# Optimization experiments

Hardware: AMD Instinct MI355X
Metric: run time of the kernel (lower is better)

The kernel has to match this reference:

```python
import jax, jax.numpy as jnp
import numpy as np

B, N, C = 8, 2048, 128
K = 16
DILATIONS = (1, 2)
KMAX = K * max(DILATIONS)  # neighbors constructed by DilatedKnnGraph
NEG_SLOPE = 0.2


def setup_inputs() -> dict:
    key = jax.random.key(0)
    ks = jax.random.split(key, 12)
    D = len(DILATIONS)

    def nrm(k, shape, fan_in):
        return jax.random.normal(k, shape, jnp.float32) / np.float32(np.sqrt(fan_in))

    x = jax.random.normal(ks[0], (B, N, C), jnp.float32)
    pos = jax.random.normal(ks[1], (B, N, 3), jnp.float32)
    # PointTransformerConv params per dilation layer (bias-free lin/lin_src/lin_dst, pos_nn=Linear(3,C))
    W_lin = nrm(ks[2], (D, C, C), C)
    W_src = nrm(ks[3], (D, C, C), C)
    W_dst = nrm(ks[4], (D, C, C), C)
    W_pos = nrm(ks[5], (D, 3, C), 3)
    b_pos = jnp.zeros((D, C), jnp.float32)
    # global fusion MLP: Linear(C+3, C) + LeakyReLU(0.2)
    Wg = nrm(ks[6], (C + 3, C), C + 3)
    bg = jnp.zeros((C,), jnp.float32)
    # final MLP: Linear(C,C) + LeakyReLU(0.2) + Linear(C,3)
    W1 = nrm(ks[7], (C, C), C)
    b1 = jnp.zeros((C,), jnp.float32)
    W2 = nrm(ks[8], (C, 3), C)
    b2 = jnp.zeros((3,), jnp.float32)
    return dict(x=x, pos=pos, W_lin=W_lin, W_src=W_src, W_dst=W_dst,
                W_pos=W_pos, b_pos=b_pos, Wg=Wg, bg=bg, W1=W1, b1=b1, W2=W2, b2=b2)


def _knn(p):
    # p: [N, 3] -> [N, KMAX] neighbor indices sorted by ascending distance (self excluded)
    sq = jnp.sum(p * p, axis=-1)
    d2 = sq[:, None] + sq[None, :] - 2.0 * (p @ p.T)
    d2 = d2 + jnp.eye(p.shape[0], dtype=p.dtype) * jnp.float32(1e10)
    _, idx = jax.lax.top_k(-d2, KMAX)
    return idx


def reference(x, pos, W_lin, W_src, W_dst, W_pos, b_pos, Wg, bg, W1, b1, W2, b2):
    nbr = jax.vmap(_knn)(pos)  # [B, N, KMAX]
    self_idx = jnp.broadcast_to(jnp.arange(N)[None, :, None], (B, N, 1))
    gather = jax.vmap(lambda arr, idx: arr[idx])  # per-cloud fancy gather

    h = None
    for li, d in enumerate(DILATIONS):
        # Dilated neighbor selection: every d-th of sorted neighbors, keep K, plus self loop
        idx = jnp.concatenate([nbr[:, :, ::d][:, :, :K], self_idx], axis=-1)  # [B, N, K+1]
        pos_j = gather(pos, idx)  # [B, N, K+1, 3]
        # delta_ij = pos_nn(pos_i - pos_j)
        delta = jnp.einsum('bnkt,tc->bnkc', pos[:, :, None, :] - pos_j, W_pos[li]) + b_pos[li]
        s = x @ W_src[li]   # lin_src
        v = x @ W_lin[li]   # value projection
        t = x @ W_dst[li]   # lin_dst
        # alpha_ij = lin_dst(x_i) - lin_src(x_j) + delta ; per-channel softmax over neighbors
        alpha = t[:, :, None, :] - gather(s, idx) + delta  # [B, N, K+1, C]
        w = jax.nn.softmax(alpha, axis=2)
        h_ = jnp.sum(w * (gather(v, idx) + delta), axis=2)  # [B, N, C]
        h = h_ if h is None else h + h_

    h2 = jax.nn.leaky_relu(jnp.concatenate([x, pos], axis=-1) @ Wg + bg, NEG_SLOPE)
    h = h + h2
    res = jax.nn.leaky_relu(h @ W1 + b1, NEG_SLOPE) @ W2 + b2
    return res + pos  # add_points=True
```

## Files before the change

kernel.cpp:

```cpp
#include <hip/hip_runtime.h>

#define BB 8
#define NN 2048
#define CC 128
#define KMAX 32
#define NEG 0.2f
#define CH 8
#define CHSZ (NN / CH)
#define CAP 32

using bf16x8 = __attribute__((ext_vector_type(8))) short;
using f32x4  = __attribute__((ext_vector_type(4))) float;

__device__ __forceinline__ unsigned int f2key(float f) {
  unsigned int b = __float_as_uint(f);
  return (b & 0x80000000u) ? ~b : (b | 0x80000000u);
}

__device__ __forceinline__ float sq3(float x, float y, float z) {
  return __fadd_rn(__fadd_rn(__fmul_rn(x, x), __fmul_rn(y, y)), __fmul_rn(z, z));
}

__device__ __forceinline__ float d2np(float px, float py, float pz, float sqq,
                                      float qx, float qy, float qz, float sqj) {
  float dot = __fmaf_rn(pz, qz, __fmaf_rn(py, qy, __fmul_rn(px, qx)));
  return __fsub_rn(__fadd_rn(sqq, sqj), __fmul_rn(2.0f, dot));
}

__device__ __forceinline__ unsigned short f2bf(float f) {
  unsigned int u = __float_as_uint(f);
  return (unsigned short)((u + 0x7fffu + ((u >> 16) & 1u)) >> 16);
}
__device__ __forceinline__ float bf2f(unsigned short u) {
  return __uint_as_float(((unsigned int)u) << 16);
}

__device__ __forceinline__ bf16x8 cvt8(const float* __restrict__ p) {
  float4 a = *(const float4*)(p);
  float4 b = *(const float4*)(p + 4);
  bf16x8 r;
  r[0] = (short)f2bf(a.x); r[1] = (short)f2bf(a.y);
  r[2] = (short)f2bf(a.z); r[3] = (short)f2bf(a.w);
  r[4] = (short)f2bf(b.x); r[5] = (short)f2bf(b.y);
  r[6] = (short)f2bf(b.z); r[7] = (short)f2bf(b.w);
  return r;
}

__device__ __forceinline__ int paddr(int c, int jj) { return (c << 8) + (jj ^ c); }

__device__ __forceinline__ void knn_body(int bx, int tid,
                                         const float* __restrict__ pos,
                                         unsigned short* __restrict__ cand,
                                         unsigned int* __restrict__ candk,
                                         float4* __restrict__ sp4,
                                         unsigned char* __restrict__ sbuf) {
  int b = bx >> 6;
  int qbase = (bx & 63) * 32;
  const float* pb = pos + (size_t)b * NN * 3;
  for (int t = tid; t < NN; t += 256) {
    float xx = pb[t * 3 + 0];
    float yy = pb[t * 3 + 1];
    float zz = pb[t * 3 + 2];
    sp4[paddr(t >> 8, t & 255)] = make_float4(xx, yy, zz, sq3(xx, yy, zz));
  }
  __syncthreads();

  int q = qbase + (tid >> 3);
  int c = tid & 7;
  float4 pq = sp4[paddr(q >> 8, q & 255)];
  float px = pq.x, py = pq.y, pz = pq.z;
  float sqq = pq.w;
  int j0 = c * CHSZ;

  const float SENT = 3.0e38f;
  float a0 = SENT, a1 = SENT, a2 = SENT, a3 = SENT;
#pragma unroll 4
  for (int jj = 0; jj < CHSZ; ++jj) {
    float4 pj = sp4[paddr(c, jj)];
    float d2 = d2np(px, py, pz, sqq, pj.x, pj.y, pj.z, pj.w);
    if (j0 + jj == q) d2 = SENT;
    float m0 = fmaxf(a0, d2); a0 = fminf(a0, d2);
    float m1 = fmaxf(a1, m0); a1 = fminf(a1, m0);
    float m2 = fmaxf(a2, m1); a2 = fminf(a2, m1);
    a3 = fminf(a3, m2);
  }

  float T = a3;
  T = fmaxf(T, __shfl_xor(T, 1));
  T = fmaxf(T, __shfl_xor(T, 2));
  T = fmaxf(T, __shfl_xor(T, 4));

  unsigned int ak[KMAX];
  int ai[KMAX];
#pragma unroll
  for (int k = 0; k < KMAX; ++k) { ak[k] = 0xFFFFFFFFu; ai[k] = 0xFFFF; }

  int sbase = tid * CAP;
  auto drain = [&](int cnt2) {
    for (int u = 0; u < cnt2; ++u) {
      int jj2 = (int)sbuf[sbase + u];
      int j = j0 + jj2;
      float4 pj = sp4[paddr(c, jj2)];
      float d2 = d2np(px, py, pz, sqq, pj.x, pj.y, pj.z, pj.w);
      unsigned int key = f2key(d2);
      if (key < ak[KMAX - 1]) {
#pragma unroll
        for (int k = KMAX - 1; k >= 1; --k) {
          bool ck  = key < ak[k];
          bool ckm = key < ak[k - 1];
          unsigned int tk = ckm ? ak[k - 1] : key;
          int          ti = ckm ? ai[k - 1] : j;
          ak[k] = ck ? tk : ak[k];
          ai[k] = ck ? ti : ai[k];
        }
        bool c0b = key < ak[0];
        ak[0] = c0b ? key : ak[0];
        ai[0] = c0b ? j : ai[0];
      }
    }
  };

  int cnt = 0;
  for (int jj = 0; jj < CHSZ; ++jj) {
    float4 pj = sp4[paddr(c, jj)];
    float d2 = d2np(px, py, pz, sqq, pj.x, pj.y, pj.z, pj.w);
    bool pass = (d2 <= T) && (j0 + jj != q);
    if (pass) {
      if (cnt == CAP) { drain(CAP); cnt = 0; }
      sbuf[sbase + cnt] = (unsigned char)jj;
      ++cnt;
    }
  }
  drain(cnt);

  size_t obase = (((size_t)(b * NN + q)) * CH + c) * KMAX;
  unsigned short* oc = cand + obase;
  unsigned int* ok = candk + obase;
#pragma unroll
  for (int k = 0; k < KMAX; ++k) {
    oc[k] = (unsigned short)ai[k];
    ok[k] = ak[k];
  }
}

__device__ __forceinline__ void proj_body(int z, int mx, int tid,
                                          const float* __restrict__ x,
                                          const unsigned short* __restrict__ wf,
                                          unsigned short* __restrict__ projb) {
  unsigned short* out = projb + (size_t)z * ((size_t)BB * NN * CC);
  int wave = tid >> 6;
  int lane = tid & 63;
  int m0 = (mx * 4 + wave) * 16;
  int quad = lane >> 4;
  int am = m0 + (lane & 15);

  f32x4 acc[8];
#pragma unroll
  for (int nt = 0; nt < 8; ++nt) acc[nt] = (f32x4){0.f, 0.f, 0.f, 0.f};

  const unsigned short* wz = wf + (size_t)z * (8 * 4 * 64 * 8);
#pragma unroll
  for (int ks = 0; ks < 4; ++ks) {
    bf16x8 a = cvt8(x + (size_t)am * CC + ks * 32 + quad * 8);
#pragma unroll
    for (int nt = 0; nt < 8; ++nt) {
      bf16x8 bfr = *(const bf16x8*)(wz + (size_t)(((nt * 4 + ks) * 64 + lane) * 8));
      acc[nt] = __builtin_amdgcn_mfma_f32_16x16x32_bf16(a, bfr, acc[nt], 0, 0, 0);
    }
  }

  int col0 = lane & 15;
#pragma unroll
  for (int nt = 0; nt < 8; ++nt)
#pragma unroll
    for (int r = 0; r < 4; ++r)
      out[(size_t)(m0 + quad * 4 + r) * CC + nt * 16 + col0] = f2bf(acc[nt][r]);
}

__device__ __forceinline__ void wg_body(int mx, int tid,
                                        const float* __restrict__ x,
                                        const float* __restrict__ pos,
                                        const unsigned short* __restrict__ wf,
                                        const float* __restrict__ wgtail,
                                        const float* __restrict__ bg,
                                        float* __restrict__ h) {
  int wave = tid >> 6;
  int lane = tid & 63;
  int m0 = (mx * 4 + wave) * 16;
  int quad = lane >> 4;
  int am = m0 + (lane & 15);

  f32x4 acc[8];
#pragma unroll
  for (int nt = 0; nt < 8; ++nt) acc[nt] = (f32x4){0.f, 0.f, 0.f, 0.f};

  const unsigned short* wz = wf + (size_t)6 * (8 * 4 * 64 * 8);
#pragma unroll
  for (int ks = 0; ks < 4; ++ks) {
    bf16x8 a = cvt8(x + (size_t)am * CC + ks * 32 + quad * 8);
#pragma unroll
    for (int nt = 0; nt < 8; ++nt) {
      bf16x8 b = *(const bf16x8*)(wz + (size_t)(((nt * 4 + ks) * 64 + lane) * 8));
      acc[nt] = __builtin_amdgcn_mfma_f32_16x16x32_bf16(a, b, acc[nt], 0, 0, 0);
    }
  }

  float posr[4][3];
#pragma unroll
  for (int r = 0; r < 4; ++r) {
    int m = m0 + quad * 4 + r;
    posr[r][0] = pos[m * 3 + 0];
    posr[r][1] = pos[m * 3 + 1];
    posr[r][2] = pos[m * 3 + 2];
  }

  int col0 = lane & 15;
#pragma unroll
  for (int nt = 0; nt < 8; ++nt) {
    int col = nt * 16 + col0;
    float bv = bg[col];
    float t0 = wgtail[col];
    float t1 = wgtail[CC + col];
    float t2 = wgtail[2 * CC + col];
#pragma unroll
    for (int r = 0; r < 4; ++r) {
      float v = acc[nt][r] + bv
              + posr[r][0] * t0 + posr[r][1] * t1 + posr[r][2] * t2;
      v = v > 0.f ? v : NEG * v;
      h[(size_t)(m0 + quad * 4 + r) * CC + col] = v;
    }
  }
}

__global__ __launch_bounds__(256) void fused_front(
    const float* __restrict__ pos,
    unsigned short* __restrict__ cand,
    unsigned int* __restrict__ candk,
    const float* __restrict__ x,
    const unsigned short* __restrict__ wf,
    unsigned short* __restrict__ projb,
    const float* __restrict__ wgtail,
    const float* __restrict__ bg,
    float* __restrict__ h) {
  __shared__ float4 sp4[CH * 256];
  __shared__ unsigned char sbuf[256 * CAP];

  if (blockIdx.x < 512) {
    knn_body(blockIdx.x, threadIdx.x, pos, cand, candk, sp4, sbuf);
  } else if (blockIdx.x < 2048) {
    int bx = blockIdx.x - 512;
    proj_body(bx >> 8, bx & 255, threadIdx.x, x, wf, projb);
  } else {
    wg_body(blockIdx.x - 2048, threadIdx.x, x, pos, wf, wgtail, bg, h);
  }
}

__global__ __launch_bounds__(256) void knn_p1(const float* __restrict__ pos,
                                              unsigned short* __restrict__ cand,
                                              unsigned int* __restrict__ candk) {
  __shared__ float4 sp4[CH * 256];
  __shared__ unsigned char sbuf[256 * CAP];
  knn_body(blockIdx.x, threadIdx.x, pos, cand, candk, sp4, sbuf);
}

__global__ __launch_bounds__(64) void knn_p2(const unsigned int* __restrict__ candk,
                                             const unsigned short* __restrict__ cand,
                                             int* __restrict__ nbr) {
  int q = blockIdx.x * 64 + threadIdx.x;
  const unsigned int* k8 = candk + (size_t)q * (CH * KMAX);
  const unsigned short* i8 = cand + (size_t)q * (CH * KMAX);

  int head[CH];
  unsigned int hk[CH];
#pragma unroll
  for (int c = 0; c < CH; ++c) {
    head[c] = 0;
    hk[c] = k8[c * KMAX];
  }

  int* onb = nbr + (size_t)q * KMAX;
#pragma unroll
  for (int r = 0; r < KMAX; ++r) {
    int bc = 0;
    unsigned int bk = hk[0];
#pragma unroll
    for (int c = 1; c < CH; ++c) {
      if (hk[c] < bk) { bk = hk[c]; bc = c; }
    }
    onb[r] = (int)i8[bc * KMAX + head[bc]];
    ++head[bc];
    hk[bc] = (head[bc] < KMAX) ? k8[bc * KMAX + head[bc]] : 0xFFFFFFFFu;
  }
}

__global__ __launch_bounds__(256) void wcvt(const float* __restrict__ Wa,
                                            const float* __restrict__ Wb,
                                            const float* __restrict__ Wc,
                                            const float* __restrict__ Wgm,
                                            const float* __restrict__ W1m,
                                            unsigned short* __restrict__ wf) {
  int t = blockIdx.x * 256 + threadIdx.x;
  int lane = t & 63;
  int ks = (t >> 6) & 3;
  int nt = (t >> 8) & 7;
  int z = t >> 11;
  const float* W = (z < 2) ? (Wa + (size_t)z * CC * CC)
                 : (z < 4) ? (Wb + (size_t)(z - 2) * CC * CC)
                 : (z < 6) ? (Wc + (size_t)(z - 4) * CC * CC)
                 : (z == 6) ? Wgm : W1m;
  int n = nt * 16 + (lane & 15);
  int kb = ks * 32 + (lane >> 4) * 8;
  unsigned short* o = wf + (size_t)t * 8;
#pragma unroll
  for (int j = 0; j < 8; ++j)
    o[j] = f2bf(W[(size_t)(kb + j) * CC + n]);
}

__global__ __launch_bounds__(256) void proj_fly(const float* __restrict__ x,
                                                const unsigned short* __restrict__ wf,
                                                unsigned short* __restrict__ projb) {
  proj_body(blockIdx.z, blockIdx.x, threadIdx.x, x, wf, projb);
}
__global__ __launch_bounds__(256) void wg_fly(const float* __restrict__ x,
                                              const float* __restrict__ pos,
                                              const unsigned short* __restrict__ wf,
                                              const float* __restrict__ wgtail,
                                              const float* __restrict__ bg,
                                              float* __restrict__ h) {
  wg_body(blockIdx.x, threadIdx.x, x, pos, wf, wgtail, bg, h);
}

__global__ __launch_bounds__(128) void attn2_kernel(
    const float* __restrict__ pos, const int* __restrict__ nbr,
    const unsigned short* __restrict__ s0, const unsigned short* __restrict__ v0,
    const unsigned short* __restrict__ t0,
    const unsigned short* __restrict__ s1, const unsigned short* __restrict__ v1,
    const unsigned short* __restrict__ t1,
    const float* __restrict__ Wpos, const float* __restrict__ bpos,
    const float* __restrict__ h, unsigned short* __restrict__ hb) {
  int b = blockIdx.x & 7;
  int n = blockIdx.x >> 3;
  int bn = (b << 11) + n;
  int c = threadIdx.x;

  const float* pb = pos + (size_t)b * NN * 3;
  float pix = pb[n * 3 + 0], piy = pb[n * 3 + 1], piz = pb[n * 3 + 2];

  const int* nb = nbr + (size_t)bn * KMAX;
  int idxs[KMAX];
#pragma unroll
  for (int u = 0; u < KMAX / 4; ++u) {
    int4 v4 = *(const int4*)(nb + u * 4);
    idxs[u * 4 + 0] = v4.x; idxs[u * 4 + 1] = v4.y;
    idxs[u * 4 + 2] = v4.z; idxs[u * 4 + 3] = v4.w;
  }

  float ht = h[(size_t)bn * CC + c];

#pragma unroll
  for (int l = 0; l < 2; ++l) {
    int dil = l + 1;
    const unsigned short* s = l ? s1 : s0;
    const unsigned short* v = l ? v1 : v0;
    const unsigned short* t = l ? t1 : t0;
    const float* Wp = Wpos + (size_t)l * 3 * CC;
    float w0 = Wp[c], w1 = Wp[CC + c], w2 = Wp[2 * CC + c];
    float bp = bpos[(size_t)l * CC + c];
    float tc = bf2f(t[(size_t)bn * CC + c]);

    int id[17];
#pragma unroll
    for (int j = 0; j < 17; ++j) id[j] = (j < 16) ? idxs[j * dil] : n;

    float sc[17];
#pragma unroll
    for (int j = 0; j < 17; ++j)
      sc[j] = bf2f(s[((size_t)(b * NN + id[j])) * CC + c]);

    float alpha[17], del[17];
#pragma unroll
    for (int j = 0; j < 17; ++j) {
      int idx = id[j];
      float dx = pix - pb[idx * 3 + 0];
      float dy = piy - pb[idx * 3 + 1];
      float dz = piz - pb[idx * 3 + 2];
      float d = dx * w0 + dy * w1 + dz * w2 + bp;
      del[j] = d;
      alpha[j] = tc - sc[j] + d;
    }
    float m8[8];
#pragma unroll
    for (int j = 0; j < 8; ++j) m8[j] = fmaxf(alpha[j], alpha[j + 8]);
    float m4a = fmaxf(m8[0], m8[1]), m4b = fmaxf(m8[2], m8[3]);
    float m4c = fmaxf(m8[4], m8[5]), m4d = fmaxf(m8[6], m8[7]);
    float mx = fmaxf(fmaxf(fmaxf(m4a, m4b), fmaxf(m4c, m4d)), alpha[16]);

    float sum = 0.f;
#pragma unroll
    for (int j = 0; j < 17; ++j) {
      float w = __expf(alpha[j] - mx);
      alpha[j] = w;
      sum += w;
    }
    float inv = 1.f / sum;

    float vc[17];
#pragma unroll
    for (int j = 0; j < 17; ++j)
      vc[j] = bf2f(v[((size_t)(b * NN + id[j])) * CC + c]);

    float hc = 0.f;
#pragma unroll
    for (int j = 0; j < 17; ++j)
      hc += alpha[j] * (vc[j] + del[j]);
    ht += hc * inv;
  }

  hb[(size_t)bn * CC + c] = f2bf(ht);
}

__global__ __launch_bounds__(256) void mfma_w1_final(
    const unsigned short* __restrict__ hb,
    const unsigned short* __restrict__ wz,
    const float* __restrict__ b1,
    const float* __restrict__ W2,
    const float* __restrict__ b2,
    const float* __restrict__ pos,
    float* __restrict__ out) {
  int wave = threadIdx.x >> 6;
  int lane = threadIdx.x & 63;
  int m0 = (blockIdx.x * 4 + wave) * 16;
  int quad = lane >> 4;
  int am = m0 + (lane & 15);

  f32x4 acc[8];
#pragma unroll
  for (int nt = 0; nt < 8; ++nt) acc[nt] = (f32x4){0.f, 0.f, 0.f, 0.f};

#pragma unroll
  for (int ks = 0; ks < 4; ++ks) {
    bf16x8 a = *(const bf16x8*)(hb + (size_t)am * CC + ks * 32 + quad * 8);
#pragma unroll
    for (int nt = 0; nt < 8; ++nt) {
      bf16x8 b = *(const bf16x8*)(wz + (size_t)(((nt * 4 + ks) * 64 + lane) * 8));
      acc[nt] = __builtin_amdgcn_mfma_f32_16x16x32_bf16(a, b, acc[nt], 0, 0, 0);
    }
  }

  int col0 = lane & 15;
  float part[4][3];
#pragma unroll
  for (int r = 0; r < 4; ++r)
#pragma unroll
    for (int d = 0; d < 3; ++d) part[r][d] = 0.f;

#pragma unroll
  for (int nt = 0; nt < 8; ++nt) {
    int col = nt * 16 + col0;
    float bv = b1[col];
    float w20 = W2[col * 3 + 0];
    float w21 = W2[col * 3 + 1];
    float w22 = W2[col * 3 + 2];
#pragma unroll
    for (int r = 0; r < 4; ++r) {
      float gv = acc[nt][r] + bv;
      gv = gv > 0.f ? gv : NEG * gv;
      part[r][0] = fmaf(gv, w20, part[r][0]);
      part[r][1] = fmaf(gv, w21, part[r][1]);
      part[r][2] = fmaf(gv, w22, part[r][2]);
    }
  }

#pragma unroll
  for (int off = 8; off >= 1; off >>= 1) {
#pragma unroll
    for (int r = 0; r < 4; ++r)
#pragma unroll
      for (int d = 0; d < 3; ++d)
        part[r][d] += __shfl_xor(part[r][d], off);
  }

  if (col0 == 0) {
#pragma unroll
    for (int r = 0; r < 4; ++r) {
      int m = m0 + quad * 4 + r;
#pragma unroll
      for (int d = 0; d < 3; ++d)
        out[(size_t)m * 3 + d] = part[r][d] + b2[d] + pos[(size_t)m * 3 + d];
    }
  }
}

extern "C" void kernel_launch(void* const* d_in, const int* in_sizes, int n_in,
                              void* d_out, int out_size, void* d_ws, size_t ws_size,
                              hipStream_t stream) {
  const float* x     = (const float*)d_in[0];
  const float* pos   = (const float*)d_in[1];
  const float* W_lin = (const float*)d_in[2];
  const float* W_src = (const float*)d_in[3];
  const float* W_dst = (const float*)d_in[4];
  const float* W_pos = (const float*)d_in[5];
  const float* b_pos = (const float*)d_in[6];
  const float* Wg    = (const float*)d_in[7];
  const float* bg    = (const float*)d_in[8];
  const float* W1    = (const float*)d_in[9];
  const float* b1    = (const float*)d_in[10];
  const float* W2    = (const float*)d_in[11];
  const float* b2    = (const float*)d_in[12];
  float* out = (float*)d_out;

  const size_t M = (size_t)BB * NN;
  const size_t MC = M * CC;

  char* ws = (char*)d_ws;
  int* nbr = (int*)ws;
  unsigned short* cand = (unsigned short*)(ws + M * KMAX * sizeof(int));
  float* fb = (float*)(ws + M * KMAX * sizeof(int) + M * CH * KMAX * sizeof(unsigned short));
  unsigned short* projb = (unsigned short*)fb;
  unsigned short* sb0 = projb + 0 * MC;
  unsigned short* sb1 = projb + 1 * MC;
  unsigned short* vb0 = projb + 2 * MC;
  unsigned short* vb1 = projb + 3 * MC;
  unsigned short* tb0 = projb + 4 * MC;
  unsigned short* tb1 = projb + 5 * MC;
  unsigned int* candk = (unsigned int*)(fb + 3 * MC);
  float* h = fb + 5 * MC;

  const size_t BASE = M * KMAX * sizeof(int) + M * CH * KMAX * sizeof(unsigned short)
                    + 8 * MC * sizeof(float);
  const size_t XB_BYTES = MC * sizeof(unsigned short);
  const size_t WF_BYTES = 8 * 16384 * sizeof(unsigned short);
  const size_t FRAG = (size_t)(8 * 4 * 64 * 8);
  bool fused_ok = ws_size >= BASE + XB_BYTES + WF_BYTES;

  if (fused_ok) {
    unsigned short* hb = (unsigned short*)(ws + BASE);
    unsigned short* wf = (unsigned short*)(ws + BASE + XB_BYTES);

    wcvt<<<64, 256, 0, stream>>>(W_src, W_lin, W_dst, Wg, W1, wf);
    fused_front<<<2304, 256, 0, stream>>>(pos, cand, candk, x, wf, projb,
                                          Wg + 128 * CC, bg, h);
    knn_p2<<<256, 64, 0, stream>>>(candk, cand, nbr);
    attn2_kernel<<<M, 128, 0, stream>>>(pos, nbr, sb0, vb0, tb0,
                                        sb1, vb1, tb1, W_pos, b_pos, h, hb);
    mfma_w1_final<<<M / 64, 256, 0, stream>>>(hb, wf + 7 * FRAG, b1,
                                              W2, b2, pos, out);
  } else {
    unsigned short* hb = cand;
    unsigned short* wf = cand + MC;
    knn_p1<<<512, 256, 0, stream>>>(pos, cand, candk);
    knn_p2<<<256, 64, 0, stream>>>(candk, cand, nbr);
    wcvt<<<64, 256, 0, stream>>>(W_src, W_lin, W_dst, Wg, W1, wf);
    proj_fly<<<dim3(256, 1, 6), 256, 0, stream>>>(x, wf, projb);
    wg_fly<<<256, 256, 0, stream>>>(x, pos, wf, Wg + 128 * CC, bg, h);
    attn2_kernel<<<M, 128, 0, stream>>>(pos, nbr, sb0, vb0, tb0,
                                        sb1, vb1, tb1, W_pos, b_pos, h, hb);
    mfma_w1_final<<<M / 64, 256, 0, stream>>>(hb, wf + 7 * FRAG, b1,
                                              W2, b2, pos, out);
  }
}
```

Baseline: 218.6 us.

## Fuse kNN candidate merge into kNN kernel and precompute per-point pos projections

The per-chunk kNN candidate lists are now merged inside the kNN block through shared memory, with one thread per query. This removes the separate knn_p2 launch and the global round-trip of the candidate keys and indices. Separately, pos@W_pos is precomputed once per point and layer into an fp32 buffer in an enlarged wcvt kernel. The attention kernel then forms delta as the difference of two gathered projection rows instead of recomputing it from three gathered coordinates. The precompute exploits linearity to drop per-edge FMAs, but it adds a 16 MB fp32 buffer and many wide per-neighbor gathers. The in-block merge runs serially on only one thread in eight.

```diff
diff --git a/kernel.cpp b/kernel.cpp
--- a/kernel.cpp
+++ b/kernel.cpp
@@ -50,8 +50,7 @@
 
 __device__ __forceinline__ void knn_body(int bx, int tid,
                                          const float* __restrict__ pos,
-                                         unsigned short* __restrict__ cand,
-                                         unsigned int* __restrict__ candk,
+                                         int* __restrict__ nbr,
                                          float4* __restrict__ sp4,
                                          unsigned char* __restrict__ sbuf) {
   int b = bx >> 6;
@@ -133,13 +132,37 @@
   }
   drain(cnt);
 
-  size_t obase = (((size_t)(b * NN + q)) * CH + c) * KMAX;
-  unsigned short* oc = cand + obase;
-  unsigned int* ok = candk + obase;
+  __syncthreads();
+  unsigned int* mkey = (unsigned int*)sp4;
+  unsigned char* mjj = sbuf;
+  int ql = tid >> 3;
+  int mbase = (ql * 8 + c) * 32;
 #pragma unroll
   for (int k = 0; k < KMAX; ++k) {
-    oc[k] = (unsigned short)ai[k];
-    ok[k] = ak[k];
+    mkey[mbase + k] = ak[k];
+    mjj[mbase + k] = (unsigned char)(ai[k] & 255);
+  }
+  __syncthreads();
+  if (c == 0) {
+    unsigned int hk[CH];
+    int hd[CH];
+#pragma unroll
+    for (int cc = 0; cc < CH; ++cc) {
+      hd[cc] = 0;
+      hk[cc] = mkey[(ql * 8 + cc) * 32];
+    }
+    int* onb = nbr + ((size_t)(b * NN + q)) * KMAX;
+    for (int r = 0; r < KMAX; ++r) {
+      int bc = 0;
+      unsigned int bk = hk[0];
+#pragma unroll
+      for (int cc = 1; cc < CH; ++cc) {
+        if (hk[cc] < bk) { bk = hk[cc]; bc = cc; }
+      }
+      onb[r] = bc * CHSZ + (int)mjj[(ql * 8 + bc) * 32 + hd[bc]];
+      ++hd[bc];
+      hk[bc] = (hd[bc] < KMAX) ? mkey[(ql * 8 + bc) * 32 + hd[bc]] : 0xFFFFFFFFu;
+    }
   }
 }
 
@@ -234,8 +257,7 @@
 
 __global__ __launch_bounds__(256) void fused_front(
     const float* __restrict__ pos,
-    unsigned short* __restrict__ cand,
-    unsigned int* __restrict__ candk,
+    int* __restrict__ nbr,
     const float* __restrict__ x,
     const unsigned short* __restrict__ wf,
     unsigned short* __restrict__ projb,
@@ -246,7 +268,7 @@
   __shared__ unsigned char sbuf[256 * CAP];
 
   if (blockIdx.x < 512) {
-    knn_body(blockIdx.x, threadIdx.x, pos, cand, candk, sp4, sbuf);
+    knn_body(blockIdx.x, threadIdx.x, pos, nbr, sp4, sbuf);
   } else if (blockIdx.x < 2048) {
     int bx = blockIdx.x - 512;
     proj_body(bx >> 8, bx & 255, threadIdx.x, x, wf, projb);
@@ -256,41 +278,10 @@
 }
 
 __global__ __launch_bounds__(256) void knn_p1(const float* __restrict__ pos,
-                                              unsigned short* __restrict__ cand,
-                                              unsigned int* __restrict__ candk) {
+                                              int* __restrict__ nbr) {
   __shared__ float4 sp4[CH * 256];
   __shared__ unsigned char sbuf[256 * CAP];
-  knn_body(blockIdx.x, threadIdx.x, pos, cand, candk, sp4, sbuf);
-}
-
-__global__ __launch_bounds__(64) void knn_p2(const unsigned int* __restrict__ candk,
-                                             const unsigned short* __restrict__ cand,
-                                             int* __restrict__ nbr) {
-  int q = blockIdx.x * 64 + threadIdx.x;
-  const unsigned int* k8 = candk + (size_t)q * (CH * KMAX);
-  const unsigned short* i8 = cand + (size_t)q * (CH * KMAX);
-
-  int head[CH];
-  unsigned int hk[CH];
-#pragma unroll
-  for (int c = 0; c < CH; ++c) {
-    head[c] = 0;
-    hk[c] = k8[c * KMAX];
-  }
-
-  int* onb = nbr + (size_t)q * KMAX;
-#pragma unroll
-  for (int r = 0; r < KMAX; ++r) {
-    int bc = 0;
-    unsigned int bk = hk[0];
-#pragma unroll
-    for (int c = 1; c < CH; ++c) {
-      if (hk[c] < bk) { bk = hk[c]; bc = c; }
-    }
-    onb[r] = (int)i8[bc * KMAX + head[bc]];
-    ++head[bc];
-    hk[bc] = (head[bc] < KMAX) ? k8[bc * KMAX + head[bc]] : 0xFFFFFFFFu;
-  }
+  knn_body(blockIdx.x, threadIdx.x, pos, nbr, sp4, sbuf);
 }
 
 __global__ __launch_bounds__(256) void wcvt(const float* __restrict__ Wa,
@@ -298,22 +289,42 @@
                                             const float* __restrict__ Wc,
                                             const float* __restrict__ Wgm,
                                             const float* __restrict__ W1m,
-                                            unsigned short* __restrict__ wf) {
-  int t = blockIdx.x * 256 + threadIdx.x;
-  int lane = t & 63;
-  int ks = (t >> 6) & 3;
-  int nt = (t >> 8) & 7;
-  int z = t >> 11;
-  const float* W = (z < 2) ? (Wa + (size_t)z * CC * CC)
-                 : (z < 4) ? (Wb + (size_t)(z - 2) * CC * CC)
-                 : (z < 6) ? (Wc + (size_t)(z - 4) * CC * CC)
-                 : (z == 6) ? Wgm : W1m;
-  int n = nt * 16 + (lane & 15);
-  int kb = ks * 32 + (lane >> 4) * 8;
-  unsigned short* o = wf + (size_t)t * 8;
-#pragma unroll
-  for (int j = 0; j < 8; ++j)
-    o[j] = f2bf(W[(size_t)(kb + j) * CC + n]);
+                                            unsigned short* __restrict__ wf,
+                                            const float* __restrict__ Wpos,
+                                            const float* __restrict__ pos,
+                                            float* __restrict__ pp) {
+  if (blockIdx.x < 64) {
+    int t = blockIdx.x * 256 + threadIdx.x;
+    int lane = t & 63;
+    int ks = (t >> 6) & 3;
+    int nt = (t >> 8) & 7;
+    int z = t >> 11;
+    const float* W = (z < 2) ? (Wa + (size_t)z * CC * CC)
+                   : (z < 4) ? (Wb + (size_t)(z - 2) * CC * CC)
+                   : (z < 6) ? (Wc + (size_t)(z - 4) * CC * CC)
+                   : (z == 6) ? Wgm : W1m;
+    int n = nt * 16 + (lane & 15);
+    int kb = ks * 32 + (lane >> 4) * 8;
+    unsigned short* o = wf + (size_t)t * 8;
+#pragma unroll
+    for (int j = 0; j < 8; ++j)
+      o[j] = f2bf(W[(size_t)(kb + j) * CC + n]);
+  } else {
+    int pb2 = blockIdx.x - 64;
+    int l = threadIdx.x >> 7;
+    int c = threadIdx.x & 127;
+    const float* Wp = Wpos + (size_t)l * 3 * CC;
+    float w0 = Wp[c], w1 = Wp[CC + c], w2 = Wp[2 * CC + c];
+    float* ppl = pp + (size_t)l * ((size_t)BB * NN * CC);
+    int m0 = pb2 * 128;
+    for (int mi = 0; mi < 128; ++mi) {
+      int m = m0 + mi;
+      float xx = pos[m * 3 + 0];
+      float yy = pos[m * 3 + 1];
+      float zz = pos[m * 3 + 2];
+      ppl[(size_t)m * CC + c] = __fmaf_rn(zz, w2, __fmaf_rn(yy, w1, __fmul_rn(xx, w0)));
+    }
+  }
 }
 
 __global__ __launch_bounds__(256) void proj_fly(const float* __restrict__ x,
@@ -331,21 +342,18 @@
 }
 
 __global__ __launch_bounds__(128) void attn2_kernel(
-    const float* __restrict__ pos, const int* __restrict__ nbr,
+    const int* __restrict__ nbr,
     const unsigned short* __restrict__ s0, const unsigned short* __restrict__ v0,
     const unsigned short* __restrict__ t0,
     const unsigned short* __restrict__ s1, const unsigned short* __restrict__ v1,
     const unsigned short* __restrict__ t1,
-    const float* __restrict__ Wpos, const float* __restrict__ bpos,
+    const float* __restrict__ pp, const float* __restrict__ bpos,
     const float* __restrict__ h, unsigned short* __restrict__ hb) {
   int b = blockIdx.x & 7;
   int n = blockIdx.x >> 3;
   int bn = (b << 11) + n;
   int c = threadIdx.x;
 
-  const float* pb = pos + (size_t)b * NN * 3;
-  float pix = pb[n * 3 + 0], piy = pb[n * 3 + 1], piz = pb[n * 3 + 2];
-
   const int* nb = nbr + (size_t)bn * KMAX;
   int idxs[KMAX];
 #pragma unroll
@@ -363,28 +371,27 @@
     const unsigned short* s = l ? s1 : s0;
     const unsigned short* v = l ? v1 : v0;
     const unsigned short* t = l ? t1 : t0;
-    const float* Wp = Wpos + (size_t)l * 3 * CC;
-    float w0 = Wp[c], w1 = Wp[CC + c], w2 = Wp[2 * CC + c];
+    const float* ppl = pp + (size_t)l * ((size_t)BB * NN * CC);
     float bp = bpos[(size_t)l * CC + c];
     float tc = bf2f(t[(size_t)bn * CC + c]);
+    float ppi = ppl[(size_t)bn * CC + c];
 
     int id[17];
 #pragma unroll
     for (int j = 0; j < 17; ++j) id[j] = (j < 16) ? idxs[j * dil] : n;
 
-    float sc[17];
+    float sc[17], pj[17];
 #pragma unroll
     for (int j = 0; j < 17; ++j)
       sc[j] = bf2f(s[((size_t)(b * NN + id[j])) * CC + c]);
+#pragma unroll
+    for (int j = 0; j < 17; ++j)
+      pj[j] = ppl[((size_t)(b * NN + id[j])) * CC + c];
 
     float alpha[17], del[17];
 #pragma unroll
     for (int j = 0; j < 17; ++j) {
-      int idx = id[j];
-      float dx = pix - pb[idx * 3 + 0];
-      float dy = piy - pb[idx * 3 + 1];
-      float dz = piz - pb[idx * 3 + 2];
-      float d = dx * w0 + dy * w1 + dz * w2 + bp;
+      float d = ppi - pj[j] + bp;
       del[j] = d;
       alpha[j] = tc - sc[j] + d;
     }
@@ -523,8 +530,8 @@
   unsigned short* vb1 = projb + 3 * MC;
   unsigned short* tb0 = projb + 4 * MC;
   unsigned short* tb1 = projb + 5 * MC;
-  unsigned int* candk = (unsigned int*)(fb + 3 * MC);
   float* h = fb + 5 * MC;
+  float* pp = fb + 6 * MC;
 
   const size_t BASE = M * KMAX * sizeof(int) + M * CH * KMAX * sizeof(unsigned short)
                     + 8 * MC * sizeof(float);
@@ -537,24 +544,22 @@
     unsigned short* hb = (unsigned short*)(ws + BASE);
     unsigned short* wf = (unsigned short*)(ws + BASE + XB_BYTES);
 
-    wcvt<<<64, 256, 0, stream>>>(W_src, W_lin, W_dst, Wg, W1, wf);
-    fused_front<<<2304, 256, 0, stream>>>(pos, cand, candk, x, wf, projb,
+    wcvt<<<192, 256, 0, stream>>>(W_src, W_lin, W_dst, Wg, W1, wf, W_pos, pos, pp);
+    fused_front<<<2304, 256, 0, stream>>>(pos, nbr, x, wf, projb,
                                           Wg + 128 * CC, bg, h);
-    knn_p2<<<256, 64, 0, stream>>>(candk, cand, nbr);
-    attn2_kernel<<<M, 128, 0, stream>>>(pos, nbr, sb0, vb0, tb0,
-                                        sb1, vb1, tb1, W_pos, b_pos, h, hb);
+    attn2_kernel<<<M, 128, 0, stream>>>(nbr, sb0, vb0, tb0,
+                                        sb1, vb1, tb1, pp, b_pos, h, hb);
     mfma_w1_final<<<M / 64, 256, 0, stream>>>(hb, wf + 7 * FRAG, b1,
                                               W2, b2, pos, out);
   } else {
     unsigned short* hb = cand;
     unsigned short* wf = cand + MC;
-    knn_p1<<<512, 256, 0, stream>>>(pos, cand, candk);
-    knn_p2<<<256, 64, 0, stream>>>(candk, cand, nbr);
-    wcvt<<<64, 256, 0, stream>>>(W_src, W_lin, W_dst, Wg, W1, wf);
+    knn_p1<<<512, 256, 0, stream>>>(pos, nbr);
+    wcvt<<<192, 256, 0, stream>>>(W_src, W_lin, W_dst, Wg, W1, wf, W_pos, pos, pp);
     proj_fly<<<dim3(256, 1, 6), 256, 0, stream>>>(x, wf, projb);
     wg_fly<<<256, 256, 0, stream>>>(x, pos, wf, Wg + 128 * CC, bg, h);
-    attn2_kernel<<<M, 128, 0, stream>>>(pos, nbr, sb0, vb0, tb0,
-                                        sb1, vb1, tb1, W_pos, b_pos, h, hb);
+    attn2_kernel<<<M, 128, 0, stream>>>(nbr, sb0, vb0, tb0,
+                                        sb1, vb1, tb1, pp, b_pos, h, hb);
     mfma_w1_final<<<M / 64, 256, 0, stream>>>(hb, wf + 7 * FRAG, b1,
                                               W2, b2, pos, out);
   }
```

Measured after the change: 214.9 us. Within noise of the previous version (-1.7%).

## Precompute per-point positional projections and gather them in attention kernel

Applied to the files above, without the earlier changes.

Uses linearity of pos_nn to precompute pos@W_pos per point and layer in fp32 inside the weight-conversion kernel (extra blocks). The attention kernel then gathers these 128-channel projections per neighbor instead of 3 position floats and computing dot products. This replaces cheap arithmetic with large fp32 gathers (17 per layer per channel), adding 16 MB writes and much more gather traffic. It also changes rounding order slightly.

```diff
diff --git a/kernel.cpp b/kernel.cpp
--- a/kernel.cpp
+++ b/kernel.cpp
@@ -298,22 +298,42 @@
                                             const float* __restrict__ Wc,
                                             const float* __restrict__ Wgm,
                                             const float* __restrict__ W1m,
-                                            unsigned short* __restrict__ wf) {
-  int t = blockIdx.x * 256 + threadIdx.x;
-  int lane = t & 63;
-  int ks = (t >> 6) & 3;
-  int nt = (t >> 8) & 7;
-  int z = t >> 11;
-  const float* W = (z < 2) ? (Wa + (size_t)z * CC * CC)
-                 : (z < 4) ? (Wb + (size_t)(z - 2) * CC * CC)
-                 : (z < 6) ? (Wc + (size_t)(z - 4) * CC * CC)
-                 : (z == 6) ? Wgm : W1m;
-  int n = nt * 16 + (lane & 15);
-  int kb = ks * 32 + (lane >> 4) * 8;
-  unsigned short* o = wf + (size_t)t * 8;
-#pragma unroll
-  for (int j = 0; j < 8; ++j)
-    o[j] = f2bf(W[(size_t)(kb + j) * CC + n]);
+                                            unsigned short* __restrict__ wf,
+                                            const float* __restrict__ Wpos,
+                                            const float* __restrict__ pos,
+                                            float* __restrict__ pp) {
+  if (blockIdx.x < 64) {
+    int t = blockIdx.x * 256 + threadIdx.x;
+    int lane = t & 63;
+    int ks = (t >> 6) & 3;
+    int nt = (t >> 8) & 7;
+    int z = t >> 11;
+    const float* W = (z < 2) ? (Wa + (size_t)z * CC * CC)
+                   : (z < 4) ? (Wb + (size_t)(z - 2) * CC * CC)
+                   : (z < 6) ? (Wc + (size_t)(z - 4) * CC * CC)
+                   : (z == 6) ? Wgm : W1m;
+    int n = nt * 16 + (lane & 15);
+    int kb = ks * 32 + (lane >> 4) * 8;
+    unsigned short* o = wf + (size_t)t * 8;
+#pragma unroll
+    for (int j = 0; j < 8; ++j)
+      o[j] = f2bf(W[(size_t)(kb + j) * CC + n]);
+  } else {
+    int pb2 = blockIdx.x - 64;
+    int l = threadIdx.x >> 7;
+    int c = threadIdx.x & 127;
+    const float* Wp = Wpos + (size_t)l * 3 * CC;
+    float w0 = Wp[c], w1 = Wp[CC + c], w2 = Wp[2 * CC + c];
+    float* ppl = pp + (size_t)l * ((size_t)BB * NN * CC);
+    int m0 = pb2 * 128;
+    for (int mi = 0; mi < 128; ++mi) {
+      int m = m0 + mi;
+      float xx = pos[m * 3 + 0];
+      float yy = pos[m * 3 + 1];
+      float zz = pos[m * 3 + 2];
+      ppl[(size_t)m * CC + c] = __fmaf_rn(zz, w2, __fmaf_rn(yy, w1, __fmul_rn(xx, w0)));
+    }
+  }
 }
 
 __global__ __launch_bounds__(256) void proj_fly(const float* __restrict__ x,
@@ -331,21 +351,18 @@
 }
 
 __global__ __launch_bounds__(128) void attn2_kernel(
-    const float* __restrict__ pos, const int* __restrict__ nbr,
+    const int* __restrict__ nbr,
     const unsigned short* __restrict__ s0, const unsigned short* __restrict__ v0,
     const unsigned short* __restrict__ t0,
     const unsigned short* __restrict__ s1, const unsigned short* __restrict__ v1,
     const unsigned short* __restrict__ t1,
-    const float* __restrict__ Wpos, const float* __restrict__ bpos,
+    const float* __restrict__ pp, const float* __restrict__ bpos,
     const float* __restrict__ h, unsigned short* __restrict__ hb) {
   int b = blockIdx.x & 7;
   int n = blockIdx.x >> 3;
   int bn = (b << 11) + n;
   int c = threadIdx.x;
 
-  const float* pb = pos + (size_t)b * NN * 3;
-  float pix = pb[n * 3 + 0], piy = pb[n * 3 + 1], piz = pb[n * 3 + 2];
-
   const int* nb = nbr + (size_t)bn * KMAX;
   int idxs[KMAX];
 #pragma unroll
@@ -363,28 +380,27 @@
     const unsigned short* s = l ? s1 : s0;
     const unsigned short* v = l ? v1 : v0;
     const unsigned short* t = l ? t1 : t0;
-    const float* Wp = Wpos + (size_t)l * 3 * CC;
-    float w0 = Wp[c], w1 = Wp[CC + c], w2 = Wp[2 * CC + c];
+    const float* ppl = pp + (size_t)l * ((size_t)BB * NN * CC);
     float bp = bpos[(size_t)l * CC + c];
     float tc = bf2f(t[(size_t)bn * CC + c]);
+    float ppi = ppl[(size_t)bn * CC + c];
 
     int id[17];
 #pragma unroll
     for (int j = 0; j < 17; ++j) id[j] = (j < 16) ? idxs[j * dil] : n;
 
-    float sc[17];
+    float sc[17], pj[17];
 #pragma unroll
     for (int j = 0; j < 17; ++j)
       sc[j] = bf2f(s[((size_t)(b * NN + id[j])) * CC + c]);
+#pragma unroll
+    for (int j = 0; j < 17; ++j)
+      pj[j] = ppl[((size_t)(b * NN + id[j])) * CC + c];
 
     float alpha[17], del[17];
 #pragma unroll
     for (int j = 0; j < 17; ++j) {
-      int idx = id[j];
-      float dx = pix - pb[idx * 3 + 0];
-      float dy = piy - pb[idx * 3 + 1];
-      float dz = piz - pb[idx * 3 + 2];
-      float d = dx * w0 + dy * w1 + dz * w2 + bp;
+      float d = ppi - pj[j] + bp;
       del[j] = d;
       alpha[j] = tc - sc[j] + d;
     }
@@ -525,6 +541,7 @@
   unsigned short* tb1 = projb + 5 * MC;
   unsigned int* candk = (unsigned int*)(fb + 3 * MC);
   float* h = fb + 5 * MC;
+  float* pp = fb + 6 * MC;
 
   const size_t BASE = M * KMAX * sizeof(int) + M * CH * KMAX * sizeof(unsigned short)
                     + 8 * MC * sizeof(float);
@@ -537,12 +554,12 @@
     unsigned short* hb = (unsigned short*)(ws + BASE);
     unsigned short* wf = (unsigned short*)(ws + BASE + XB_BYTES);
 
-    wcvt<<<64, 256, 0, stream>>>(W_src, W_lin, W_dst, Wg, W1, wf);
+    wcvt<<<192, 256, 0, stream>>>(W_src, W_lin, W_dst, Wg, W1, wf, W_pos, pos, pp);
     fused_front<<<2304, 256, 0, stream>>>(pos, cand, candk, x, wf, projb,
                                           Wg + 128 * CC, bg, h);
     knn_p2<<<256, 64, 0, stream>>>(candk, cand, nbr);
-    attn2_kernel<<<M, 128, 0, stream>>>(pos, nbr, sb0, vb0, tb0,
-                                        sb1, vb1, tb1, W_pos, b_pos, h, hb);
+    attn2_kernel<<<M, 128, 0, stream>>>(nbr, sb0, vb0, tb0,
+                                        sb1, vb1, tb1, pp, b_pos, h, hb);
     mfma_w1_final<<<M / 64, 256, 0, stream>>>(hb, wf + 7 * FRAG, b1,
                                               W2, b2, pos, out);
   } else {
@@ -550,11 +567,11 @@
     unsigned short* wf = cand + MC;
     knn_p1<<<512, 256, 0, stream>>>(pos, cand, candk);
     knn_p2<<<256, 64, 0, stream>>>(candk, cand, nbr);
-    wcvt<<<64, 256, 0, stream>>>(W_src, W_lin, W_dst, Wg, W1, wf);
+    wcvt<<<192, 256, 0, stream>>>(W_src, W_lin, W_dst, Wg, W1, wf, W_pos, pos, pp);
     proj_fly<<<dim3(256, 1, 6), 256, 0, stream>>>(x, wf, projb);
     wg_fly<<<256, 256, 0, stream>>>(x, pos, wf, Wg + 128 * CC, bg, h);
-    attn2_kernel<<<M, 128, 0, stream>>>(pos, nbr, sb0, vb0, tb0,
-                                        sb1, vb1, tb1, W_pos, b_pos, h, hb);
+    attn2_kernel<<<M, 128, 0, stream>>>(nbr, sb0, vb0, tb0,
+                                        sb1, vb1, tb1, pp, b_pos, h, hb);
     mfma_w1_final<<<M / 64, 256, 0, stream>>>(hb, wf + 7 * FRAG, b1,
                                               W2, b2, pos, out);
   }
```

Result: no change. 220.4 us (+0.8%).
